# Optimization experiments

Hardware: AMD Instinct MI355X
Metric: run time of the kernel (lower is better)

Reference implementation:

```python
import jax, jax.numpy as jnp
import numpy as np

B, D, H = 524288, 128, 64  # batch, input_dim, hidden_dim; mask_dim = transform_dim = D//2 = 64


def _mlp(x, Wh, bh, Wo, bo):
    """eqx.nn.MLP with depth=3: 3 hidden relu layers then linear out.
    x: [B, in]; Wh: [3, H, in/H]; bh: [3, H]; Wo: [out, H]; bo: [out]."""
    h = x
    for i in range(Wh.shape[0]):  # fixed small layer loop
        h = jax.nn.relu(h @ Wh[i].T + bh[i])
    return h @ Wo.T + bo


def setup_inputs() -> dict:
    key = jax.random.key(0)
    ks = jax.random.split(key, 9)
    m = D // 2
    s = 1.0 / np.sqrt(H)  # lecun-ish init scale
    inp = {"x": jax.random.normal(ks[0], (B, D), dtype=jnp.float32)}
    inp["cond_Wh"] = jax.random.normal(ks[1], (3, H, m), dtype=jnp.float32) * s
    inp["cond_bh"] = jnp.zeros((3, H), dtype=jnp.float32)
    inp["cond_Wo"] = jax.random.normal(ks[2], (D - m, H), dtype=jnp.float32) * s
    inp["cond_bo"] = jnp.zeros((D - m,), dtype=jnp.float32)
    inp["scale_Wh"] = jax.random.normal(ks[3], (3, H, m), dtype=jnp.float32) * s
    inp["scale_bh"] = jnp.zeros((3, H), dtype=jnp.float32)
    inp["scale_Wo"] = jax.random.normal(ks[4], (D - m, H), dtype=jnp.float32) * s
    inp["scale_bo"] = jnp.zeros((D - m,), dtype=jnp.float32)
    return inp


def reference(x, cond_Wh, cond_bh, cond_Wo, cond_bo,
              scale_Wh, scale_bh, scale_Wo, scale_bo):
    m = x.shape[-1] // 2
    # mask = [1]*m + [0]*(D-m) -> mask_idx = [:m], transform_idx = [m:] (static contiguous split)
    x_masked = x[..., :m]
    x_transform = x[..., m:]
    shift = _mlp(x_masked, cond_Wh, cond_bh, cond_Wo, cond_bo)        # [B, D-m]
    log_scale = _mlp(x_masked, scale_Wh, scale_bh, scale_Wo, scale_bo)  # [B, D-m]
    scale = jnp.exp(jnp.clip(log_scale, -5, 3))
    y_transform = x_transform * scale + shift
    y = jnp.concatenate([x_masked, y_transform], axis=-1)  # scatter back (contiguous)
    logdet = jnp.sum(log_scale, axis=-1)  # note: unclipped log_scale, as in original
    return y, logdet
```

## Files before the change

kernel.cpp:

```cpp
#include <hip/hip_runtime.h>
#include <cstdint>

typedef __attribute__((ext_vector_type(8))) _Float16 half8;
typedef __attribute__((ext_vector_type(4))) _Float16 half4;
typedef __attribute__((ext_vector_type(4))) float f32x4;
typedef __attribute__((ext_vector_type(4))) unsigned int u32x4;

__global__ void prep_weights(const float* __restrict__ cWh, const float* __restrict__ cWo,
                             const float* __restrict__ sWh, const float* __restrict__ sWo,
                             const float* __restrict__ cbh, const float* __restrict__ cbo,
                             const float* __restrict__ sbh, const float* __restrict__ sbo,
                             char* __restrict__ img) {
    int t = blockIdx.x * 256 + threadIdx.x;
    if (t < 32768) {
        int e = t & 7, mt = (t >> 3) & 3, lane = (t >> 5) & 63, kp = (t >> 11) & 1, L = (t >> 12) & 7;
        const float* src = (L < 3)  ? cWh + L * 4096
                         : (L == 3) ? cWo
                         : (L < 7)  ? sWh + (L - 4) * 4096
                         :            sWo;
        int m = mt * 16 + (lane & 15);
        int k = (2 * kp + (e >> 2)) * 16 + 4 * (lane >> 4) + (e & 3);
        float w = src[m * 64 + k];
        _Float16 hi = (_Float16)w;
        _Float16 lo = (_Float16)(w - (float)hi);
        _Float16* wf = (_Float16*)img;
        int fi = (L * 2 + kp) * 2;
        wf[((fi * 4 + mt) * 64 + lane) * 8 + e]       = hi;
        wf[(((fi + 1) * 4 + mt) * 64 + lane) * 8 + e] = lo;
    } else if (t < 33280) {
        int b = t - 32768;
        int L = b >> 6, f = b & 63;
        const float* src = (L < 3)  ? cbh + L * 64
                         : (L == 3) ? cbo
                         : (L < 7)  ? sbh + (L - 4) * 64
                         :            sbo;
        ((float*)(img + 131072))[b] = src[f];
    }
}

template<bool RELU>
__device__ __forceinline__ half8 cvt_frag(f32x4 a, f32x4 b) {
    half8 r;
#pragma unroll
    for (int i = 0; i < 4; ++i) {
        float va = RELU ? fmaxf(a[i], 0.f) : a[i];
        float vb = RELU ? fmaxf(b[i], 0.f) : b[i];
        r[i]     = (_Float16)va;
        r[i + 4] = (_Float16)vb;
    }
    return r;
}

__device__ __forceinline__ void run_layer(const _Float16* __restrict__ lwf,
                                          const float* __restrict__ lb, int Lid,
                                          int lane, int g4,
                                          const half8 B[2][4], f32x4 acc[4][4]) {
#pragma unroll
    for (int mt = 0; mt < 4; ++mt) {
        f32x4 bb = *(const f32x4*)(lb + Lid * 64 + mt * 16 + g4);
#pragma unroll
        for (int nt = 0; nt < 4; ++nt) acc[mt][nt] = bb;
    }
#pragma unroll
    for (int kp = 0; kp < 2; ++kp) {
        const int fi = (Lid * 2 + kp) * 2;
        half8 Ah[4], Al[4];
#pragma unroll
        for (int mt = 0; mt < 4; ++mt) {
            Ah[mt] = *(const half8*)(lwf + ((fi * 4 + mt) * 64 + lane) * 8);
            Al[mt] = *(const half8*)(lwf + (((fi + 1) * 4 + mt) * 64 + lane) * 8);
        }
#pragma unroll
        for (int nt = 0; nt < 4; ++nt)
#pragma unroll
            for (int mt = 0; mt < 4; ++mt) {
                acc[mt][nt] = __builtin_amdgcn_mfma_f32_16x16x32_f16(Ah[mt], B[kp][nt], acc[mt][nt], 0, 0, 0);
                acc[mt][nt] = __builtin_amdgcn_mfma_f32_16x16x32_f16(Al[mt], B[kp][nt], acc[mt][nt], 0, 0, 0);
            }
    }
}

__device__ __forceinline__ void acc_to_B_relu(const f32x4 acc[4][4], half8 B[2][4]) {
#pragma unroll
    for (int kp = 0; kp < 2; ++kp)
#pragma unroll
        for (int nt = 0; nt < 4; ++nt)
            B[kp][nt] = cvt_frag<true>(acc[2 * kp][nt], acc[2 * kp + 1][nt]);
}

__global__ __launch_bounds__(512, 2)
void coupling_main(const float* __restrict__ x, const char* __restrict__ img,
                   float* __restrict__ y, float* __restrict__ logdet) {
    extern __shared__ char smem[];
    const int lane = threadIdx.x & 63;
    const int wid = threadIdx.x >> 6;
    const int c = lane & 15;
    const int g4 = (lane >> 4) * 4;
    const long row0 = (long)blockIdx.x * 512 + wid * 64;
    const float* xr = x + (row0 + c) * 128 + g4;
    float* yr = y + (row0 + c) * 128 + g4;

    f32x4 xm[4][4], xtf[4][4];
#pragma unroll
    for (int nt = 0; nt < 4; ++nt)
#pragma unroll
        for (int kt = 0; kt < 4; ++kt)
            xm[nt][kt] = *(const f32x4*)(xr + nt * 2048 + kt * 16);
#pragma unroll
    for (int nt = 0; nt < 4; ++nt)
#pragma unroll
        for (int kt = 0; kt < 4; ++kt)
            xtf[nt][kt] = *(const f32x4*)(xr + nt * 2048 + 64 + kt * 16);

    {
        const u32x4* s = (const u32x4*)img;
        u32x4* d = (u32x4*)smem;
        for (int i = threadIdx.x; i < 8320; i += 512) d[i] = s[i];
    }
    __syncthreads();
    const _Float16* lwf = (const _Float16*)smem;
    const float* lb = (const float*)(smem + 131072);

    half8 B0[2][4];
#pragma unroll
    for (int nt = 0; nt < 4; ++nt) {
#pragma unroll
        for (int kt = 0; kt < 4; ++kt)
            __builtin_nontemporal_store(xm[nt][kt], (f32x4*)(yr + nt * 2048 + kt * 16));
        B0[0][nt] = cvt_frag<false>(xm[nt][0], xm[nt][1]);
        B0[1][nt] = cvt_frag<false>(xm[nt][2], xm[nt][3]);
    }
    half8 xth[4][2];
#pragma unroll
    for (int nt = 0; nt < 4; ++nt) {
        xth[nt][0] = cvt_frag<false>(xtf[nt][0], xtf[nt][1]);
        xth[nt][1] = cvt_frag<false>(xtf[nt][2], xtf[nt][3]);
    }

    f32x4 acc[4][4];
    half8 B[2][4];

    run_layer(lwf, lb, 0, lane, g4, B0, acc);
    acc_to_B_relu(acc, B);
    run_layer(lwf, lb, 1, lane, g4, B, acc);
    acc_to_B_relu(acc, B);
    run_layer(lwf, lb, 2, lane, g4, B, acc);
    acc_to_B_relu(acc, B);
    run_layer(lwf, lb, 3, lane, g4, B, acc);
    half4 shp[4][4];
#pragma unroll
    for (int mt = 0; mt < 4; ++mt)
#pragma unroll
        for (int nt = 0; nt < 4; ++nt) {
            half4 s;
#pragma unroll
            for (int i = 0; i < 4; ++i) s[i] = (_Float16)acc[mt][nt][i];
            shp[mt][nt] = s;
        }

    run_layer(lwf, lb, 4, lane, g4, B0, acc);
    acc_to_B_relu(acc, B);
    run_layer(lwf, lb, 5, lane, g4, B, acc);
    acc_to_B_relu(acc, B);
    run_layer(lwf, lb, 6, lane, g4, B, acc);
    acc_to_B_relu(acc, B);
    run_layer(lwf, lb, 7, lane, g4, B, acc);

    float pld0 = 0.f, pld1 = 0.f, pld2 = 0.f, pld3 = 0.f;
#pragma unroll
    for (int nt = 0; nt < 4; ++nt) {
        float psum = 0.f;
#pragma unroll
        for (int mt = 0; mt < 4; ++mt) {
            f32x4 ls = acc[mt][nt];
            psum += ls[0] + ls[1] + ls[2] + ls[3];
            half8 xh = xth[nt][mt >> 1];
            const int o4 = (mt & 1) * 4;
            half4 sp = shp[mt][nt];
            f32x4 o;
#pragma unroll
            for (int i = 0; i < 4; ++i) {
                float cl = fminf(fmaxf(ls[i], -5.f), 3.f);
                o[i] = (float)xh[o4 + i] * __expf(cl) + (float)sp[i];
            }
            __builtin_nontemporal_store(o, (f32x4*)(yr + nt * 2048 + 64 + mt * 16));
        }
        if (nt == 0) pld0 = psum; else if (nt == 1) pld1 = psum;
        else if (nt == 2) pld2 = psum; else pld3 = psum;
    }
#pragma unroll
    for (int nt = 0; nt < 4; ++nt) {
        float v = (nt == 0) ? pld0 : (nt == 1) ? pld1 : (nt == 2) ? pld2 : pld3;
        v += __shfl_xor(v, 16);
        v += __shfl_xor(v, 32);
        if ((lane >> 4) == 0) logdet[row0 + nt * 16 + c] = v;
    }
}

extern "C" void kernel_launch(void* const* d_in, const int* in_sizes, int n_in,
                              void* d_out, int out_size, void* d_ws, size_t ws_size,
                              hipStream_t stream) {
    const float* x   = (const float*)d_in[0];
    const float* cWh = (const float*)d_in[1];
    const float* cbh = (const float*)d_in[2];
    const float* cWo = (const float*)d_in[3];
    const float* cbo = (const float*)d_in[4];
    const float* sWh = (const float*)d_in[5];
    const float* sbh = (const float*)d_in[6];
    const float* sWo = (const float*)d_in[7];
    const float* sbo = (const float*)d_in[8];

    const int B = in_sizes[0] / 128;
    const int LDS_BYTES = 133120;

    char* img = (char*)d_ws;

    prep_weights<<<130, 256, 0, stream>>>(cWh, cWo, sWh, sWo, cbh, cbo, sbh, sbo, img);

    (void)hipFuncSetAttribute((const void*)coupling_main,
                              hipFuncAttributeMaxDynamicSharedMemorySize, LDS_BYTES);

    float* y = (float*)d_out;
    float* logdet = y + (size_t)B * 128;
    coupling_main<<<B / 512, 512, LDS_BYTES, stream>>>(x, img, y, logdet);
}
```

Baseline: 193.6 us.

## Make main kernel persistent with software-prefetched x tiles across iterations

Switches from one block per 512 rows to 256 persistent blocks that each loop over 8 tiles of 256 rows (32 rows per wave). The weight image is loaded into LDS once per block and reused across all tiles, and the next tile's x is loaded into registers while the current tile's MLP runs. This aims to remove repeated 130KB LDS fills and hide global load latency behind MFMA work. Halving rows per wave lowers per-tile parallelism, and the grid size and tile stride are now hardcoded to B=524288.

```diff
diff --git a/kernel.cpp b/kernel.cpp
--- a/kernel.cpp
+++ b/kernel.cpp
@@ -54,12 +54,12 @@
 __device__ __forceinline__ void run_layer(const _Float16* __restrict__ lwf,
                                           const float* __restrict__ lb, int Lid,
                                           int lane, int g4,
-                                          const half8 B[2][4], f32x4 acc[4][4]) {
+                                          const half8 B[2][2], f32x4 acc[4][2]) {
 #pragma unroll
     for (int mt = 0; mt < 4; ++mt) {
         f32x4 bb = *(const f32x4*)(lb + Lid * 64 + mt * 16 + g4);
 #pragma unroll
-        for (int nt = 0; nt < 4; ++nt) acc[mt][nt] = bb;
+        for (int nt = 0; nt < 2; ++nt) acc[mt][nt] = bb;
     }
 #pragma unroll
     for (int kp = 0; kp < 2; ++kp) {
@@ -71,7 +71,7 @@
             Al[mt] = *(const half8*)(lwf + (((fi + 1) * 4 + mt) * 64 + lane) * 8);
         }
 #pragma unroll
-        for (int nt = 0; nt < 4; ++nt)
+        for (int nt = 0; nt < 2; ++nt)
 #pragma unroll
             for (int mt = 0; mt < 4; ++mt) {
                 acc[mt][nt] = __builtin_amdgcn_mfma_f32_16x16x32_f16(Ah[mt], B[kp][nt], acc[mt][nt], 0, 0, 0);
@@ -80,120 +80,131 @@
     }
 }
 
-__device__ __forceinline__ void acc_to_B_relu(const f32x4 acc[4][4], half8 B[2][4]) {
+__device__ __forceinline__ void acc_to_B_relu(const f32x4 acc[4][2], half8 B[2][2]) {
 #pragma unroll
     for (int kp = 0; kp < 2; ++kp)
 #pragma unroll
-        for (int nt = 0; nt < 4; ++nt)
+        for (int nt = 0; nt < 2; ++nt)
             B[kp][nt] = cvt_frag<true>(acc[2 * kp][nt], acc[2 * kp + 1][nt]);
 }
 
+#define NTILES 8
+#define TILE_ROW_STRIDE (256L * 256L)
 __global__ __launch_bounds__(512, 2)
 void coupling_main(const float* __restrict__ x, const char* __restrict__ img,
                    float* __restrict__ y, float* __restrict__ logdet) {
     extern __shared__ char smem[];
+    {
+        const u32x4* s = (const u32x4*)img;
+        u32x4* d = (u32x4*)smem;
+        for (int i = threadIdx.x; i < 8320; i += 512) d[i] = s[i];
+    }
     const int lane = threadIdx.x & 63;
     const int wid = threadIdx.x >> 6;
     const int c = lane & 15;
     const int g4 = (lane >> 4) * 4;
-    const long row0 = (long)blockIdx.x * 512 + wid * 64;
-    const float* xr = x + (row0 + c) * 128 + g4;
-    float* yr = y + (row0 + c) * 128 + g4;
-
-    f32x4 xm[4][4], xtf[4][4];
-#pragma unroll
-    for (int nt = 0; nt < 4; ++nt)
-#pragma unroll
-        for (int kt = 0; kt < 4; ++kt)
-            xm[nt][kt] = *(const f32x4*)(xr + nt * 2048 + kt * 16);
-#pragma unroll
-    for (int nt = 0; nt < 4; ++nt)
-#pragma unroll
-        for (int kt = 0; kt < 4; ++kt)
-            xtf[nt][kt] = *(const f32x4*)(xr + nt * 2048 + 64 + kt * 16);
-
+    const long row0 = (long)blockIdx.x * 256 + wid * 32;
+
+    f32x4 xm[2][4], xt[2][4];
     {
-        const u32x4* s = (const u32x4*)img;
-        u32x4* d = (u32x4*)smem;
-        for (int i = threadIdx.x; i < 8320; i += 512) d[i] = s[i];
+        const float* xr = x + (row0 + c) * 128 + g4;
+#pragma unroll
+        for (int nt = 0; nt < 2; ++nt)
+#pragma unroll
+            for (int kt = 0; kt < 4; ++kt) {
+                xm[nt][kt] = *(const f32x4*)(xr + nt * 2048 + kt * 16);
+                xt[nt][kt] = *(const f32x4*)(xr + nt * 2048 + 64 + kt * 16);
+            }
     }
     __syncthreads();
     const _Float16* lwf = (const _Float16*)smem;
     const float* lb = (const float*)(smem + 131072);
 
-    half8 B0[2][4];
-#pragma unroll
-    for (int nt = 0; nt < 4; ++nt) {
-#pragma unroll
-        for (int kt = 0; kt < 4; ++kt)
-            __builtin_nontemporal_store(xm[nt][kt], (f32x4*)(yr + nt * 2048 + kt * 16));
-        B0[0][nt] = cvt_frag<false>(xm[nt][0], xm[nt][1]);
-        B0[1][nt] = cvt_frag<false>(xm[nt][2], xm[nt][3]);
-    }
-    half8 xth[4][2];
-#pragma unroll
-    for (int nt = 0; nt < 4; ++nt) {
-        xth[nt][0] = cvt_frag<false>(xtf[nt][0], xtf[nt][1]);
-        xth[nt][1] = cvt_frag<false>(xtf[nt][2], xtf[nt][3]);
-    }
-
-    f32x4 acc[4][4];
-    half8 B[2][4];
-
-    run_layer(lwf, lb, 0, lane, g4, B0, acc);
-    acc_to_B_relu(acc, B);
-    run_layer(lwf, lb, 1, lane, g4, B, acc);
-    acc_to_B_relu(acc, B);
-    run_layer(lwf, lb, 2, lane, g4, B, acc);
-    acc_to_B_relu(acc, B);
-    run_layer(lwf, lb, 3, lane, g4, B, acc);
-    half4 shp[4][4];
-#pragma unroll
-    for (int mt = 0; mt < 4; ++mt)
-#pragma unroll
-        for (int nt = 0; nt < 4; ++nt) {
-            half4 s;
-#pragma unroll
-            for (int i = 0; i < 4; ++i) s[i] = (_Float16)acc[mt][nt][i];
-            shp[mt][nt] = s;
-        }
-
-    run_layer(lwf, lb, 4, lane, g4, B0, acc);
-    acc_to_B_relu(acc, B);
-    run_layer(lwf, lb, 5, lane, g4, B, acc);
-    acc_to_B_relu(acc, B);
-    run_layer(lwf, lb, 6, lane, g4, B, acc);
-    acc_to_B_relu(acc, B);
-    run_layer(lwf, lb, 7, lane, g4, B, acc);
-
-    float pld0 = 0.f, pld1 = 0.f, pld2 = 0.f, pld3 = 0.f;
-#pragma unroll
-    for (int nt = 0; nt < 4; ++nt) {
-        float psum = 0.f;
-#pragma unroll
-        for (int mt = 0; mt < 4; ++mt) {
-            f32x4 ls = acc[mt][nt];
-            psum += ls[0] + ls[1] + ls[2] + ls[3];
-            half8 xh = xth[nt][mt >> 1];
-            const int o4 = (mt & 1) * 4;
-            half4 sp = shp[mt][nt];
-            f32x4 o;
-#pragma unroll
-            for (int i = 0; i < 4; ++i) {
-                float cl = fminf(fmaxf(ls[i], -5.f), 3.f);
-                o[i] = (float)xh[o4 + i] * __expf(cl) + (float)sp[i];
-            }
-            __builtin_nontemporal_store(o, (f32x4*)(yr + nt * 2048 + 64 + mt * 16));
-        }
-        if (nt == 0) pld0 = psum; else if (nt == 1) pld1 = psum;
-        else if (nt == 2) pld2 = psum; else pld3 = psum;
-    }
-#pragma unroll
-    for (int nt = 0; nt < 4; ++nt) {
-        float v = (nt == 0) ? pld0 : (nt == 1) ? pld1 : (nt == 2) ? pld2 : pld3;
-        v += __shfl_xor(v, 16);
-        v += __shfl_xor(v, 32);
-        if ((lane >> 4) == 0) logdet[row0 + nt * 16 + c] = v;
+    for (int t = 0; t < NTILES; ++t) {
+        const long r0 = row0 + (long)t * TILE_ROW_STRIDE;
+        const float* xr = x + (r0 + c) * 128 + g4;
+        float* yr = y + (r0 + c) * 128 + g4;
+
+        half8 B0[2][2], xth[2][2];
+#pragma unroll
+        for (int nt = 0; nt < 2; ++nt) {
+#pragma unroll
+            for (int kt = 0; kt < 4; ++kt)
+                __builtin_nontemporal_store(xm[nt][kt], (f32x4*)(yr + nt * 2048 + kt * 16));
+            B0[0][nt]  = cvt_frag<false>(xm[nt][0], xm[nt][1]);
+            B0[1][nt]  = cvt_frag<false>(xm[nt][2], xm[nt][3]);
+            xth[nt][0] = cvt_frag<false>(xt[nt][0], xt[nt][1]);
+            xth[nt][1] = cvt_frag<false>(xt[nt][2], xt[nt][3]);
+        }
+
+        if (t + 1 < NTILES) {
+            const float* xrn = xr + TILE_ROW_STRIDE * 128;
+#pragma unroll
+            for (int nt = 0; nt < 2; ++nt)
+#pragma unroll
+                for (int kt = 0; kt < 4; ++kt) {
+                    xm[nt][kt] = *(const f32x4*)(xrn + nt * 2048 + kt * 16);
+                    xt[nt][kt] = *(const f32x4*)(xrn + nt * 2048 + 64 + kt * 16);
+                }
+        }
+
+        f32x4 acc[4][2];
+        half8 B[2][2];
+
+        run_layer(lwf, lb, 0, lane, g4, B0, acc);
+        acc_to_B_relu(acc, B);
+        run_layer(lwf, lb, 1, lane, g4, B, acc);
+        acc_to_B_relu(acc, B);
+        run_layer(lwf, lb, 2, lane, g4, B, acc);
+        acc_to_B_relu(acc, B);
+        run_layer(lwf, lb, 3, lane, g4, B, acc);
+        half4 shp[4][2];
+#pragma unroll
+        for (int mt = 0; mt < 4; ++mt)
+#pragma unroll
+            for (int nt = 0; nt < 2; ++nt) {
+                half4 s;
+#pragma unroll
+                for (int i = 0; i < 4; ++i) s[i] = (_Float16)acc[mt][nt][i];
+                shp[mt][nt] = s;
+            }
+
+        run_layer(lwf, lb, 4, lane, g4, B0, acc);
+        acc_to_B_relu(acc, B);
+        run_layer(lwf, lb, 5, lane, g4, B, acc);
+        acc_to_B_relu(acc, B);
+        run_layer(lwf, lb, 6, lane, g4, B, acc);
+        acc_to_B_relu(acc, B);
+        run_layer(lwf, lb, 7, lane, g4, B, acc);
+
+        float pld0 = 0.f, pld1 = 0.f;
+#pragma unroll
+        for (int nt = 0; nt < 2; ++nt) {
+            float psum = 0.f;
+#pragma unroll
+            for (int mt = 0; mt < 4; ++mt) {
+                f32x4 ls = acc[mt][nt];
+                psum += ls[0] + ls[1] + ls[2] + ls[3];
+                half8 xh = xth[nt][mt >> 1];
+                const int o4 = (mt & 1) * 4;
+                half4 sp = shp[mt][nt];
+                f32x4 o;
+#pragma unroll
+                for (int i = 0; i < 4; ++i) {
+                    float cl = fminf(fmaxf(ls[i], -5.f), 3.f);
+                    o[i] = (float)xh[o4 + i] * __expf(cl) + (float)sp[i];
+                }
+                __builtin_nontemporal_store(o, (f32x4*)(yr + nt * 2048 + 64 + mt * 16));
+            }
+            if (nt == 0) pld0 = psum; else pld1 = psum;
+        }
+#pragma unroll
+        for (int nt = 0; nt < 2; ++nt) {
+            float v = (nt == 0) ? pld0 : pld1;
+            v += __shfl_xor(v, 16);
+            v += __shfl_xor(v, 32);
+            if ((lane >> 4) == 0) logdet[r0 + nt * 16 + c] = v;
+        }
     }
 }
 
@@ -222,5 +233,5 @@
 
     float* y = (float*)d_out;
     float* logdet = y + (size_t)B * 128;
-    coupling_main<<<B / 512, 512, LDS_BYTES, stream>>>(x, img, y, logdet);
-}
+    coupling_main<<<256, 512, LDS_BYTES, stream>>>(x, img, y, logdet);
+}
```

Result: slower. 695.7 us (+259.4%).
